# Kernel optimization log

Hardware: AMD Instinct MI355X
Metric: run time of the kernel (lower is better)

## Reference

```python
import jax, jax.numpy as jnp
import numpy as np

TAGSET = 50
T = TAGSET + 2      # tag_size incl START/STOP
START = T - 2       # START_TAG = -2
STOP = T - 1        # STOP_TAG = -1
NEG = -10000.0
B, S = 1024, 512


def _constrain(feats):
    # emissions to START/STOP are forbidden
    return feats.at[..., START].set(NEG).at[..., STOP].set(NEG)


def setup_inputs() -> dict:
    key = jax.random.key(0)
    kf, kl, kt, ktr = jax.random.split(key, 4)
    feats = jax.random.normal(kf, (B, S, T), jnp.float32)
    lengths = jax.random.randint(kl, (B,), S // 4, S + 1)
    mask = jnp.arange(S)[None, :] < lengths[:, None]  # bool prefix mask [B,S]
    tags = jax.random.randint(kt, (B, S), 0, TAGSET)
    # learned param: transitions with START/STOP constraints (as reset_parameters, but random base)
    transitions = 0.1 * jax.random.normal(ktr, (T, T), jnp.float32)
    transitions = transitions.at[:, START].set(NEG).at[STOP, :].set(NEG)
    return {"feats": feats, "mask": mask, "tags": tags, "transitions": transitions}


def reference(feats, mask, tags, transitions):
    del tags  # not used by Viterbi decode (forward)
    feats = _constrain(feats)
    b, s, t = feats.shape
    maskb = mask.astype(bool)
    lengths = jnp.maximum(maskb.sum(axis=1), 1)  # [B]

    alpha0 = transitions[START][None, :] + feats[:, 0]  # [B,T]

    def vstep(alpha, xs):
        f_t, m_t = xs  # [B,T], [B]
        scores = alpha[:, :, None] + transitions[None, :, :] + f_t[:, None, :]  # [B,T_prev,T_cur]
        nxt = scores.max(axis=1)
        bp = scores.argmax(axis=1).astype(jnp.int32)  # [B,T]
        alpha = jnp.where(m_t[:, None], nxt, alpha)
        return alpha, bp

    alpha, history = jax.lax.scan(
        vstep, alpha0, (feats[:, 1:].transpose(1, 0, 2), maskb[:, 1:].T)
    )  # history: [S-1,B,T]

    best_last = jnp.argmax(alpha + transitions[:, STOP][None, :], axis=1).astype(jnp.int32)  # [B]

    # pad so hist_pad[pos] == history[pos-1] for pos>=1
    hist_pad = jnp.concatenate([jnp.zeros((1, b, t), jnp.int32), history], axis=0)  # [S,B,T]

    def tb(ptr, xs):
        pos, bp = xs  # scalar, [B,T]
        ptr = jnp.where(pos == lengths - 1, best_last, ptr)
        tag = jnp.where(pos <= lengths - 1, ptr, 0)  # positions past length stay 0
        nxt = jnp.take_along_axis(bp, ptr[:, None], axis=1)[:, 0]
        ptr = jnp.where((pos >= 1) & (pos <= lengths - 1), nxt, ptr)
        return ptr, tag

    _, decoded = jax.lax.scan(tb, best_last, (jnp.arange(s), hist_pad), reverse=True)  # [S,B]
    return decoded.T  # [B,S] int32 best path
```

## Files before the change

kernel.cpp:

```cpp
#include <hip/hip_runtime.h>

#define TT 52
#define NT 50
#define START_TAG 50
#define STOP_TAG 51
#define BB 1024
#define SS 512
#define BPSTR 64

__device__ __forceinline__ int seq_len(const void* mask, int b, int j) {
    int cnt = 0;
    const unsigned* w = (const unsigned*)mask;
    unsigned w0 = w[0];
    unsigned w1 = w[1];
    if (w0 == 0x01010101u) {
        const unsigned char* m = (const unsigned char*)mask + (size_t)b * SS;
        for (int k = j; k < SS; k += 64) cnt += (m[k] != 0);
    } else if (w0 == 0x3f800000u) {
        const float* m = (const float*)mask + (size_t)b * SS;
        for (int k = j; k < SS; k += 64) cnt += (m[k] != 0.f);
    } else if (w1 == 1u) {
        const int* m = (const int*)mask + (size_t)b * SS;
        for (int k = j; k < SS; k += 64) cnt += (m[k] != 0);
    } else {
        const long long* m = (const long long*)mask + (size_t)b * SS;
        for (int k = j; k < SS; k += 64) cnt += (m[k] != 0);
    }
    for (int off = 32; off; off >>= 1) cnt += __shfl_xor(cnt, off, 64);
    return cnt > 0 ? cnt : 1;
}

#define DP_STEP(FREG, POSV)                                                       \
    {                                                                             \
        a_sh[(POSV) & 1][j] = alpha;                                              \
        float q_[52];                                                             \
        _Pragma("unroll")                                                         \
        for (int r_ = 0; r_ < 13; ++r_) {                                         \
            float4 t4_ = ((const float4*)a_sh[(POSV) & 1])[r_];                   \
            q_[4 * r_ + 0] = t4_.x; q_[4 * r_ + 1] = t4_.y;                       \
            q_[4 * r_ + 2] = t4_.z; q_[4 * r_ + 3] = t4_.w;                       \
        }                                                                         \
        float s_[NT];                                                             \
        _Pragma("unroll")                                                         \
        for (int i_ = 0; i_ < NT; ++i_) s_[i_] = q_[i_] + tt[i_];                 \
        float m_[17];                                                             \
        _Pragma("unroll")                                                         \
        for (int k_ = 0; k_ < 16; ++k_)                                           \
            m_[k_] = fmaxf(fmaxf(s_[3 * k_], s_[3 * k_ + 1]), s_[3 * k_ + 2]);    \
        m_[16] = fmaxf(s_[48], s_[49]);                                           \
        float n_[6];                                                              \
        _Pragma("unroll")                                                         \
        for (int k_ = 0; k_ < 5; ++k_)                                            \
            n_[k_] = fmaxf(fmaxf(m_[3 * k_], m_[3 * k_ + 1]), m_[3 * k_ + 2]);    \
        n_[5] = fmaxf(m_[15], m_[16]);                                            \
        float q0_ = fmaxf(fmaxf(n_[0], n_[1]), n_[2]);                            \
        float q1_ = fmaxf(fmaxf(n_[3], n_[4]), n_[5]);                            \
        float bv_ = fmaxf(q0_, q1_);                                              \
        wsb[(size_t)(POSV) * 64] = bv_;                                           \
        alpha = bv_ + (FREG);                                                     \
    }

#define FLD(P) fp[(size_t)((P) < SS ? (P) : SS - 1) * TT]

__global__ __launch_bounds__(64, 1) void crf_viterbi_fast(
    const float* __restrict__ feats,
    const void*  __restrict__ mask,
    const float* __restrict__ trans,
    float* __restrict__ ws,
    int* __restrict__ out)
{
    __shared__ float trans_lds[64 * 53];
    __shared__ __align__(16) float a_sh[2][64];

    const int b = blockIdx.x;
    const int j = threadIdx.x;
    const int jc = j < NT ? j : NT - 1;
    const int jr = j * 53;

    for (int k = j; k < 64 * 53; k += 64) {
        int r = k / 53, c = k - r * 53;
        float v = -3.0e38f;
        if (r < NT && c < TT) v = trans[r * TT + c];
        trans_lds[k] = v;
    }

    const int len = seq_len(mask, b, j);

    float tt[NT];
#pragma unroll
    for (int i = 0; i < NT; ++i) tt[i] = trans[i * TT + j];

    const float* fp = feats + ((size_t)b * SS) * TT + jc;
    float* wsb = ws + ((size_t)b * SS) * 64 + j;
    const float bv0 = trans[START_TAG * TT + jc];
    float alpha = bv0 + fp[0];
    wsb[0] = bv0;

    float fA0 = FLD(1), fA1 = FLD(2), fA2 = FLD(3), fA3 = FLD(4);
    float fB0 = FLD(5), fB1 = FLD(6), fB2 = FLD(7), fB3 = FLD(8);

    int pos = 1;
    for (; pos + 7 < len; pos += 8) {
        DP_STEP(fA0, pos + 0)
        DP_STEP(fA1, pos + 1)
        DP_STEP(fA2, pos + 2)
        DP_STEP(fA3, pos + 3)
        fA0 = FLD(pos + 8);  fA1 = FLD(pos + 9);
        fA2 = FLD(pos + 10); fA3 = FLD(pos + 11);
        DP_STEP(fB0, pos + 4)
        DP_STEP(fB1, pos + 5)
        DP_STEP(fB2, pos + 6)
        DP_STEP(fB3, pos + 7)
        fB0 = FLD(pos + 12); fB1 = FLD(pos + 13);
        fB2 = FLD(pos + 14); fB3 = FLD(pos + 15);
    }
    if (pos < len) { DP_STEP(fA0, pos) ++pos; }
    if (pos < len) { DP_STEP(fA1, pos) ++pos; }
    if (pos < len) { DP_STEP(fA2, pos) ++pos; }
    if (pos < len) { DP_STEP(fA3, pos) ++pos; }
    if (pos < len) { DP_STEP(fB0, pos) ++pos; }
    if (pos < len) { DP_STEP(fB1, pos) ++pos; }
    if (pos < len) { DP_STEP(fB2, pos) ++pos; }

    float v = alpha + trans[jc * TT + STOP_TAG];
    if (j >= NT) v = -3.0e38f;
    int idxb = j < NT ? j : 0;
    for (int off = 32; off; off >>= 1) {
        float vo = __shfl_xor(v, off, 64);
        int   io = __shfl_xor(idxb, off, 64);
        if (vo > v || (vo == v && io < idxb)) { v = vo; idxb = io; }
    }

    __syncthreads();

    int ptr = idxb;
    int* ob = out + (size_t)b * SS;
    ob[len - 1] = ptr;

    const float* wsr = ws + ((size_t)b * SS) * 64;
    const float* fbase = feats + ((size_t)b * SS) * TT;

    float bvs[4], fs[4];
    float bv_cur;
    {
        int r0 = len - 1;
        bv_cur = wsr[(size_t)r0 * 64 + j];
#pragma unroll
        for (int k = 0; k < 4; ++k) {
            int r = len - 2 - k; int rc = r < 0 ? 0 : r;
            bvs[k] = wsr[(size_t)rc * 64 + j];
            fs[k]  = fbase[(size_t)rc * TT + jc];
        }
    }

    int tpos = len - 1;

#define TB_STEP(k)                                                              \
    {                                                                           \
        float bv_prev = bvs[k];                                                 \
        float alpha_prev = bv_prev + fs[k];                                     \
        float cand = alpha_prev + trans_lds[jr + ptr];                          \
        float candm = (j < NT) ? cand : -3.0e38f;                               \
        float tgt = __builtin_bit_cast(float,                                   \
            __builtin_amdgcn_readlane(__builtin_bit_cast(int, bv_cur), ptr));   \
        unsigned long long bm = __ballot(candm == tgt);                         \
        ptr = __ffsll(bm) - 1;                                                  \
        --tpos;                                                                 \
        ob[tpos] = ptr;                                                         \
        bv_cur = bv_prev;                                                       \
        int rc = tpos - 4; rc = rc < 0 ? 0 : rc;                                \
        bvs[k] = wsr[(size_t)rc * 64 + j];                                      \
        fs[k]  = fbase[(size_t)rc * TT + jc];                                   \
    }

    while (tpos >= 4) {
        TB_STEP(0) TB_STEP(1) TB_STEP(2) TB_STEP(3)
    }
#pragma unroll
    for (int k = 0; k < 3; ++k) {
        if (tpos >= 1) TB_STEP(k)
    }
#undef TB_STEP

    for (int p = len + j; p < SS; p += 64) ob[p] = 0;
}

__global__ __launch_bounds__(64, 1) void crf_viterbi(
    const float* __restrict__ feats,
    const void*  __restrict__ mask,
    const float* __restrict__ trans,
    int* __restrict__ out)
{
    __shared__ unsigned char bp_sh[SS * BPSTR];

    const int b = blockIdx.x;
    const int j = threadIdx.x;
    const int jc = j < NT ? j : NT - 1;

    const int len = seq_len(mask, b, j);

    float tt[NT];
#pragma unroll
    for (int i = 0; i < NT; ++i) tt[i] = trans[i * TT + j];

    const float* fp = feats + ((size_t)b * SS) * TT + jc;
    float alpha = trans[START_TAG * TT + jc] + fp[0];
    float fnext = fp[TT];

    for (int pos = 1; pos < len; ++pos) {
        const float f = fnext;
        { int np = pos + 1 < SS ? pos + 1 : SS - 1; fnext = fp[(size_t)np * TT]; }

        float best[4] = { -3.0e38f, -3.0e38f, -3.0e38f, -3.0e38f };
        int   bidx[4] = { 0, 0, 0, 0 };
        const int abits = __builtin_bit_cast(int, alpha);
#pragma unroll
        for (int i = 0; i < NT; ++i) {
            int ab = __builtin_amdgcn_readlane(abits, i);
            float s = __builtin_bit_cast(float, ab) + tt[i];
            const int c = i & 3;
            if (s > best[c]) { best[c] = s; bidx[c] = i; }
        }
        float bv = best[0]; int bi = bidx[0];
        if (best[1] > bv || (best[1] == bv && bidx[1] < bi)) { bv = best[1]; bi = bidx[1]; }
        if (best[2] > bv || (best[2] == bv && bidx[2] < bi)) { bv = best[2]; bi = bidx[2]; }
        if (best[3] > bv || (best[3] == bv && bidx[3] < bi)) { bv = best[3]; bi = bidx[3]; }

        alpha = bv + f;
        bp_sh[pos * BPSTR + j] = (unsigned char)bi;
    }

    float v = alpha + trans[jc * TT + STOP_TAG];
    if (j >= NT) v = -3.0e38f;
    int idx = j < NT ? j : 0;
    for (int off = 32; off; off >>= 1) {
        float vo = __shfl_xor(v, off, 64);
        int   io = __shfl_xor(idx, off, 64);
        if (vo > v || (vo == v && io < idx)) { v = vo; idx = io; }
    }

    __syncthreads();

    int ptr = idx;
    int* ob = out + (size_t)b * SS;
    for (int pos = len - 1; pos >= 1; --pos) {
        if (j == 0) ob[pos] = ptr;
        ptr = (int)bp_sh[pos * BPSTR + ptr];
    }
    if (j == 0) ob[0] = ptr;

    for (int p = len + j; p < SS; p += 64) ob[p] = 0;
}

extern "C" void kernel_launch(void* const* d_in, const int* in_sizes, int n_in,
                              void* d_out, int out_size, void* d_ws, size_t ws_size,
                              hipStream_t stream) {
    const float* feats = (const float*)d_in[0];
    const void*  mask  = d_in[1];
    const float* trans = (const float*)d_in[3];
    int* out = (int*)d_out;

    const size_t need = (size_t)BB * SS * 64 * sizeof(float);
    if (ws_size >= need) {
        crf_viterbi_fast<<<dim3(BB), dim3(64), 0, stream>>>(feats, mask, trans,
                                                            (float*)d_ws, out);
    } else {
        crf_viterbi<<<dim3(BB), dim3(64), 0, stream>>>(feats, mask, trans, out);
    }
}
```

Baseline: 170.7 us.

## Sort sequences by length and interleave two Viterbi chains per wavefront

Adds a length-computation kernel and a counting-sort rank kernel, then a new Viterbi kernel in which each 64-lane block processes two sequences of similar length, interleaving their DP and traceback steps. The goal is to hide the latency of the serial per-step dependency chain (LDS round trip, max tree, readlane/ballot) by giving the wave two independent chains, and to halve the block count while balancing work through length pairing. It costs two extra small launches, including a single-block serial prefix scan, plus higher register pressure from duplicated state. It also removes a __syncthreads before traceback.

```diff
diff --git a/kernel.cpp b/kernel.cpp
--- a/kernel.cpp
+++ b/kernel.cpp
@@ -30,13 +30,13 @@
     return cnt > 0 ? cnt : 1;
 }
 
-#define DP_STEP(FREG, POSV)                                                       \
+#define DP_STEP(ALPHA, ABUF, WSB, FREG, POSV)                                     \
     {                                                                             \
-        a_sh[(POSV) & 1][j] = alpha;                                              \
+        (ABUF)[j] = ALPHA;                                                        \
         float q_[52];                                                             \
         _Pragma("unroll")                                                         \
         for (int r_ = 0; r_ < 13; ++r_) {                                         \
-            float4 t4_ = ((const float4*)a_sh[(POSV) & 1])[r_];                   \
+            float4 t4_ = ((const float4*)(ABUF))[r_];                             \
             q_[4 * r_ + 0] = t4_.x; q_[4 * r_ + 1] = t4_.y;                       \
             q_[4 * r_ + 2] = t4_.z; q_[4 * r_ + 3] = t4_.w;                       \
         }                                                                         \
@@ -56,13 +56,233 @@
         float q0_ = fmaxf(fmaxf(n_[0], n_[1]), n_[2]);                            \
         float q1_ = fmaxf(fmaxf(n_[3], n_[4]), n_[5]);                            \
         float bv_ = fmaxf(q0_, q1_);                                              \
-        wsb[(size_t)(POSV) * 64] = bv_;                                           \
-        alpha = bv_ + (FREG);                                                     \
-    }
-
-#define FLD(P) fp[(size_t)((P) < SS ? (P) : SS - 1) * TT]
-
-__global__ __launch_bounds__(64, 1) void crf_viterbi_fast(
+        (WSB)[(size_t)(POSV) * 64] = bv_;                                         \
+        ALPHA = bv_ + (FREG);                                                     \
+    }
+
+#define TB_STEP_G(PTR, TPOS, BVC, BVS, FS, OB, WSR, FB, K)                        \
+    {                                                                             \
+        float bvp_ = BVS[K];                                                      \
+        float ap_ = bvp_ + FS[K];                                                 \
+        float cand_ = ap_ + trans_lds[jr + PTR];                                  \
+        float cm_ = (j < NT) ? cand_ : -3.0e38f;                                  \
+        float tgt_ = __builtin_bit_cast(float,                                    \
+            __builtin_amdgcn_readlane(__builtin_bit_cast(int, BVC), PTR));        \
+        unsigned long long bm_ = __ballot(cm_ == tgt_);                           \
+        PTR = __ffsll(bm_) - 1;                                                   \
+        --TPOS;                                                                   \
+        OB[TPOS] = PTR;                                                           \
+        BVC = bvp_;                                                               \
+        int rc_ = TPOS - 4; rc_ = rc_ < 0 ? 0 : rc_;                              \
+        BVS[K] = WSR[(size_t)rc_ * 64 + j];                                       \
+        FS[K] = FB[(size_t)rc_ * TT + jc];                                        \
+    }
+
+__global__ __launch_bounds__(64, 1) void crf_lens(
+    const void* __restrict__ mask, int* __restrict__ lens_g)
+{
+    int len = seq_len(mask, blockIdx.x, threadIdx.x);
+    if (threadIdx.x == 0) lens_g[blockIdx.x] = len;
+}
+
+__global__ __launch_bounds__(1024, 1) void crf_rank(
+    const int* __restrict__ lens_g, int* __restrict__ perm)
+{
+    __shared__ int hist[SS + 1];
+    const int t = threadIdx.x;
+    if (t <= SS) hist[t] = 0;
+    __syncthreads();
+    const int myl = lens_g[t];
+    atomicAdd(&hist[myl], 1);
+    __syncthreads();
+    if (t == 0) {
+        int acc = 0;
+        for (int k = 0; k <= SS; ++k) { int h = hist[k]; hist[k] = acc; acc += h; }
+    }
+    __syncthreads();
+    int r = atomicAdd(&hist[myl], 1);
+    perm[r] = t;
+}
+
+__global__ __launch_bounds__(64, 1) void crf_viterbi_fast2(
+    const float* __restrict__ feats,
+    const float* __restrict__ trans,
+    const int*  __restrict__ lens_g,
+    const int*  __restrict__ perm,
+    float* __restrict__ ws,
+    int* __restrict__ out)
+{
+    __shared__ float trans_lds[64 * 53];
+    __shared__ __align__(16) float a_sh0[2][64];
+    __shared__ __align__(16) float a_sh1[2][64];
+
+    const int bid = blockIdx.x;
+    const int j = threadIdx.x;
+    const int jc = j < NT ? j : NT - 1;
+    const int jr = j * 53;
+
+    const int b0 = perm[2 * bid];
+    const int b1 = perm[2 * bid + 1];
+    const int len0 = lens_g[b0];
+    const int len1 = lens_g[b1];
+    const int lmin = len0 < len1 ? len0 : len1;
+
+    for (int k = j; k < 64 * 53; k += 64) {
+        int r = k / 53, c = k - r * 53;
+        float v = -3.0e38f;
+        if (r < NT && c < TT) v = trans[r * TT + c];
+        trans_lds[k] = v;
+    }
+
+    float tt[NT];
+#pragma unroll
+    for (int i = 0; i < NT; ++i) tt[i] = trans[i * TT + j];
+
+    const float* fp0 = feats + ((size_t)b0 * SS) * TT + jc;
+    const float* fp1 = feats + ((size_t)b1 * SS) * TT + jc;
+    float* wsb0 = ws + ((size_t)b0 * SS) * 64 + j;
+    float* wsb1 = ws + ((size_t)b1 * SS) * 64 + j;
+
+    const float bvi = trans[START_TAG * TT + jc];
+    float alpha0 = bvi + fp0[0];
+    float alpha1 = bvi + fp1[0];
+    wsb0[0] = bvi;
+    wsb1[0] = bvi;
+
+#define FLD0(P) fp0[(size_t)((P) < SS ? (P) : SS - 1) * TT]
+#define FLD1(P) fp1[(size_t)((P) < SS ? (P) : SS - 1) * TT]
+
+    float fA00 = FLD0(1), fA01 = FLD0(2), fA02 = FLD0(3), fA03 = FLD0(4);
+    float fB00 = FLD0(5), fB01 = FLD0(6), fB02 = FLD0(7), fB03 = FLD0(8);
+    float fA10 = FLD1(1), fA11 = FLD1(2), fA12 = FLD1(3), fA13 = FLD1(4);
+    float fB10 = FLD1(5), fB11 = FLD1(6), fB12 = FLD1(7), fB13 = FLD1(8);
+
+    int pos = 1;
+    for (; pos + 7 < lmin; pos += 8) {
+        DP_STEP(alpha0, a_sh0[(pos + 0) & 1], wsb0, fA00, pos + 0)
+        DP_STEP(alpha1, a_sh1[(pos + 0) & 1], wsb1, fA10, pos + 0)
+        DP_STEP(alpha0, a_sh0[(pos + 1) & 1], wsb0, fA01, pos + 1)
+        DP_STEP(alpha1, a_sh1[(pos + 1) & 1], wsb1, fA11, pos + 1)
+        DP_STEP(alpha0, a_sh0[(pos + 2) & 1], wsb0, fA02, pos + 2)
+        DP_STEP(alpha1, a_sh1[(pos + 2) & 1], wsb1, fA12, pos + 2)
+        DP_STEP(alpha0, a_sh0[(pos + 3) & 1], wsb0, fA03, pos + 3)
+        DP_STEP(alpha1, a_sh1[(pos + 3) & 1], wsb1, fA13, pos + 3)
+        fA00 = FLD0(pos + 8);  fA01 = FLD0(pos + 9);
+        fA02 = FLD0(pos + 10); fA03 = FLD0(pos + 11);
+        fA10 = FLD1(pos + 8);  fA11 = FLD1(pos + 9);
+        fA12 = FLD1(pos + 10); fA13 = FLD1(pos + 11);
+        DP_STEP(alpha0, a_sh0[(pos + 4) & 1], wsb0, fB00, pos + 4)
+        DP_STEP(alpha1, a_sh1[(pos + 4) & 1], wsb1, fB10, pos + 4)
+        DP_STEP(alpha0, a_sh0[(pos + 5) & 1], wsb0, fB01, pos + 5)
+        DP_STEP(alpha1, a_sh1[(pos + 5) & 1], wsb1, fB11, pos + 5)
+        DP_STEP(alpha0, a_sh0[(pos + 6) & 1], wsb0, fB02, pos + 6)
+        DP_STEP(alpha1, a_sh1[(pos + 6) & 1], wsb1, fB12, pos + 6)
+        DP_STEP(alpha0, a_sh0[(pos + 7) & 1], wsb0, fB03, pos + 7)
+        DP_STEP(alpha1, a_sh1[(pos + 7) & 1], wsb1, fB13, pos + 7)
+        fB00 = FLD0(pos + 12); fB01 = FLD0(pos + 13);
+        fB02 = FLD0(pos + 14); fB03 = FLD0(pos + 15);
+        fB10 = FLD1(pos + 12); fB11 = FLD1(pos + 13);
+        fB12 = FLD1(pos + 14); fB13 = FLD1(pos + 15);
+    }
+    if (pos < lmin) { DP_STEP(alpha0, a_sh0[pos & 1], wsb0, fA00, pos)
+                      DP_STEP(alpha1, a_sh1[pos & 1], wsb1, fA10, pos) ++pos; }
+    if (pos < lmin) { DP_STEP(alpha0, a_sh0[pos & 1], wsb0, fA01, pos)
+                      DP_STEP(alpha1, a_sh1[pos & 1], wsb1, fA11, pos) ++pos; }
+    if (pos < lmin) { DP_STEP(alpha0, a_sh0[pos & 1], wsb0, fA02, pos)
+                      DP_STEP(alpha1, a_sh1[pos & 1], wsb1, fA12, pos) ++pos; }
+    if (pos < lmin) { DP_STEP(alpha0, a_sh0[pos & 1], wsb0, fA03, pos)
+                      DP_STEP(alpha1, a_sh1[pos & 1], wsb1, fA13, pos) ++pos; }
+    if (pos < lmin) { DP_STEP(alpha0, a_sh0[pos & 1], wsb0, fB00, pos)
+                      DP_STEP(alpha1, a_sh1[pos & 1], wsb1, fB10, pos) ++pos; }
+    if (pos < lmin) { DP_STEP(alpha0, a_sh0[pos & 1], wsb0, fB01, pos)
+                      DP_STEP(alpha1, a_sh1[pos & 1], wsb1, fB11, pos) ++pos; }
+    if (pos < lmin) { DP_STEP(alpha0, a_sh0[pos & 1], wsb0, fB02, pos)
+                      DP_STEP(alpha1, a_sh1[pos & 1], wsb1, fB12, pos) ++pos; }
+
+    for (int p = pos; p < len0; ++p) {
+        float f = fp0[(size_t)p * TT];
+        DP_STEP(alpha0, a_sh0[p & 1], wsb0, f, p)
+    }
+    for (int p = pos; p < len1; ++p) {
+        float f = fp1[(size_t)p * TT];
+        DP_STEP(alpha1, a_sh1[p & 1], wsb1, f, p)
+    }
+
+    float v0 = alpha0 + trans[jc * TT + STOP_TAG];
+    float v1 = alpha1 + trans[jc * TT + STOP_TAG];
+    if (j >= NT) { v0 = -3.0e38f; v1 = -3.0e38f; }
+    int idx0 = j < NT ? j : 0;
+    int idx1 = idx0;
+    for (int off = 32; off; off >>= 1) {
+        float vo0 = __shfl_xor(v0, off, 64);
+        int   io0 = __shfl_xor(idx0, off, 64);
+        if (vo0 > v0 || (vo0 == v0 && io0 < idx0)) { v0 = vo0; idx0 = io0; }
+        float vo1 = __shfl_xor(v1, off, 64);
+        int   io1 = __shfl_xor(idx1, off, 64);
+        if (vo1 > v1 || (vo1 == v1 && io1 < idx1)) { v1 = vo1; idx1 = io1; }
+    }
+
+    int ptr0 = idx0, ptr1 = idx1;
+    int* ob0 = out + (size_t)b0 * SS;
+    int* ob1 = out + (size_t)b1 * SS;
+    ob0[len0 - 1] = ptr0;
+    ob1[len1 - 1] = ptr1;
+
+    const float* wsr0 = ws + ((size_t)b0 * SS) * 64;
+    const float* wsr1 = ws + ((size_t)b1 * SS) * 64;
+    const float* fb0 = feats + ((size_t)b0 * SS) * TT;
+    const float* fb1 = feats + ((size_t)b1 * SS) * TT;
+
+    float bvs0[4], fs0[4], bvs1[4], fs1[4];
+    float bvc0 = wsr0[(size_t)(len0 - 1) * 64 + j];
+    float bvc1 = wsr1[(size_t)(len1 - 1) * 64 + j];
+#pragma unroll
+    for (int k = 0; k < 4; ++k) {
+        int r0 = len0 - 2 - k; int rc0 = r0 < 0 ? 0 : r0;
+        bvs0[k] = wsr0[(size_t)rc0 * 64 + j];
+        fs0[k]  = fb0[(size_t)rc0 * TT + jc];
+        int r1 = len1 - 2 - k; int rc1 = r1 < 0 ? 0 : r1;
+        bvs1[k] = wsr1[(size_t)rc1 * 64 + j];
+        fs1[k]  = fb1[(size_t)rc1 * TT + jc];
+    }
+
+    int tpos0 = len0 - 1, tpos1 = len1 - 1;
+    while (tpos0 >= 4 && tpos1 >= 4) {
+        TB_STEP_G(ptr0, tpos0, bvc0, bvs0, fs0, ob0, wsr0, fb0, 0)
+        TB_STEP_G(ptr1, tpos1, bvc1, bvs1, fs1, ob1, wsr1, fb1, 0)
+        TB_STEP_G(ptr0, tpos0, bvc0, bvs0, fs0, ob0, wsr0, fb0, 1)
+        TB_STEP_G(ptr1, tpos1, bvc1, bvs1, fs1, ob1, wsr1, fb1, 1)
+        TB_STEP_G(ptr0, tpos0, bvc0, bvs0, fs0, ob0, wsr0, fb0, 2)
+        TB_STEP_G(ptr1, tpos1, bvc1, bvs1, fs1, ob1, wsr1, fb1, 2)
+        TB_STEP_G(ptr0, tpos0, bvc0, bvs0, fs0, ob0, wsr0, fb0, 3)
+        TB_STEP_G(ptr1, tpos1, bvc1, bvs1, fs1, ob1, wsr1, fb1, 3)
+    }
+    while (tpos0 >= 4) {
+        TB_STEP_G(ptr0, tpos0, bvc0, bvs0, fs0, ob0, wsr0, fb0, 0)
+        TB_STEP_G(ptr0, tpos0, bvc0, bvs0, fs0, ob0, wsr0, fb0, 1)
+        TB_STEP_G(ptr0, tpos0, bvc0, bvs0, fs0, ob0, wsr0, fb0, 2)
+        TB_STEP_G(ptr0, tpos0, bvc0, bvs0, fs0, ob0, wsr0, fb0, 3)
+    }
+    while (tpos1 >= 4) {
+        TB_STEP_G(ptr1, tpos1, bvc1, bvs1, fs1, ob1, wsr1, fb1, 0)
+        TB_STEP_G(ptr1, tpos1, bvc1, bvs1, fs1, ob1, wsr1, fb1, 1)
+        TB_STEP_G(ptr1, tpos1, bvc1, bvs1, fs1, ob1, wsr1, fb1, 2)
+        TB_STEP_G(ptr1, tpos1, bvc1, bvs1, fs1, ob1, wsr1, fb1, 3)
+    }
+    if (tpos0 >= 1) TB_STEP_G(ptr0, tpos0, bvc0, bvs0, fs0, ob0, wsr0, fb0, 0)
+    if (tpos0 >= 1) TB_STEP_G(ptr0, tpos0, bvc0, bvs0, fs0, ob0, wsr0, fb0, 1)
+    if (tpos0 >= 1) TB_STEP_G(ptr0, tpos0, bvc0, bvs0, fs0, ob0, wsr0, fb0, 2)
+    if (tpos1 >= 1) TB_STEP_G(ptr1, tpos1, bvc1, bvs1, fs1, ob1, wsr1, fb1, 0)
+    if (tpos1 >= 1) TB_STEP_G(ptr1, tpos1, bvc1, bvs1, fs1, ob1, wsr1, fb1, 1)
+    if (tpos1 >= 1) TB_STEP_G(ptr1, tpos1, bvc1, bvs1, fs1, ob1, wsr1, fb1, 2)
+
+    for (int p = len0 + j; p < SS; p += 64) ob0[p] = 0;
+    for (int p = len1 + j; p < SS; p += 64) ob1[p] = 0;
+#undef FLD0
+#undef FLD1
+}
+
+__global__ __launch_bounds__(64, 1) void crf_viterbi_fast1(
     const float* __restrict__ feats,
     const void*  __restrict__ mask,
     const float* __restrict__ trans,
@@ -92,35 +312,37 @@
 
     const float* fp = feats + ((size_t)b * SS) * TT + jc;
     float* wsb = ws + ((size_t)b * SS) * 64 + j;
-    const float bv0 = trans[START_TAG * TT + jc];
-    float alpha = bv0 + fp[0];
-    wsb[0] = bv0;
-
+    const float bvi = trans[START_TAG * TT + jc];
+    float alpha = bvi + fp[0];
+    wsb[0] = bvi;
+
+#define FLD(P) fp[(size_t)((P) < SS ? (P) : SS - 1) * TT]
     float fA0 = FLD(1), fA1 = FLD(2), fA2 = FLD(3), fA3 = FLD(4);
     float fB0 = FLD(5), fB1 = FLD(6), fB2 = FLD(7), fB3 = FLD(8);
 
     int pos = 1;
     for (; pos + 7 < len; pos += 8) {
-        DP_STEP(fA0, pos + 0)
-        DP_STEP(fA1, pos + 1)
-        DP_STEP(fA2, pos + 2)
-        DP_STEP(fA3, pos + 3)
+        DP_STEP(alpha, a_sh[(pos + 0) & 1], wsb, fA0, pos + 0)
+        DP_STEP(alpha, a_sh[(pos + 1) & 1], wsb, fA1, pos + 1)
+        DP_STEP(alpha, a_sh[(pos + 2) & 1], wsb, fA2, pos + 2)
+        DP_STEP(alpha, a_sh[(pos + 3) & 1], wsb, fA3, pos + 3)
         fA0 = FLD(pos + 8);  fA1 = FLD(pos + 9);
         fA2 = FLD(pos + 10); fA3 = FLD(pos + 11);
-        DP_STEP(fB0, pos + 4)
-        DP_STEP(fB1, pos + 5)
-        DP_STEP(fB2, pos + 6)
-        DP_STEP(fB3, pos + 7)
+        DP_STEP(alpha, a_sh[(pos + 4) & 1], wsb, fB0, pos + 4)
+        DP_STEP(alpha, a_sh[(pos + 5) & 1], wsb, fB1, pos + 5)
+        DP_STEP(alpha, a_sh[(pos + 6) & 1], wsb, fB2, pos + 6)
+        DP_STEP(alpha, a_sh[(pos + 7) & 1], wsb, fB3, pos + 7)
         fB0 = FLD(pos + 12); fB1 = FLD(pos + 13);
         fB2 = FLD(pos + 14); fB3 = FLD(pos + 15);
     }
-    if (pos < len) { DP_STEP(fA0, pos) ++pos; }
-    if (pos < len) { DP_STEP(fA1, pos) ++pos; }
-    if (pos < len) { DP_STEP(fA2, pos) ++pos; }
-    if (pos < len) { DP_STEP(fA3, pos) ++pos; }
-    if (pos < len) { DP_STEP(fB0, pos) ++pos; }
-    if (pos < len) { DP_STEP(fB1, pos) ++pos; }
-    if (pos < len) { DP_STEP(fB2, pos) ++pos; }
+    if (pos < len) { DP_STEP(alpha, a_sh[pos & 1], wsb, fA0, pos) ++pos; }
+    if (pos < len) { DP_STEP(alpha, a_sh[pos & 1], wsb, fA1, pos) ++pos; }
+    if (pos < len) { DP_STEP(alpha, a_sh[pos & 1], wsb, fA2, pos) ++pos; }
+    if (pos < len) { DP_STEP(alpha, a_sh[pos & 1], wsb, fA3, pos) ++pos; }
+    if (pos < len) { DP_STEP(alpha, a_sh[pos & 1], wsb, fB0, pos) ++pos; }
+    if (pos < len) { DP_STEP(alpha, a_sh[pos & 1], wsb, fB1, pos) ++pos; }
+    if (pos < len) { DP_STEP(alpha, a_sh[pos & 1], wsb, fB2, pos) ++pos; }
+#undef FLD
 
     float v = alpha + trans[jc * TT + STOP_TAG];
     if (j >= NT) v = -3.0e38f;
@@ -131,8 +353,6 @@
         if (vo > v || (vo == v && io < idxb)) { v = vo; idxb = io; }
     }
 
-    __syncthreads();
-
     int ptr = idxb;
     int* ob = out + (size_t)b * SS;
     ob[len - 1] = ptr;
@@ -141,46 +361,24 @@
     const float* fbase = feats + ((size_t)b * SS) * TT;
 
     float bvs[4], fs[4];
-    float bv_cur;
-    {
-        int r0 = len - 1;
-        bv_cur = wsr[(size_t)r0 * 64 + j];
-#pragma unroll
-        for (int k = 0; k < 4; ++k) {
-            int r = len - 2 - k; int rc = r < 0 ? 0 : r;
-            bvs[k] = wsr[(size_t)rc * 64 + j];
-            fs[k]  = fbase[(size_t)rc * TT + jc];
-        }
+    float bvc = wsr[(size_t)(len - 1) * 64 + j];
+#pragma unroll
+    for (int k = 0; k < 4; ++k) {
+        int r = len - 2 - k; int rc = r < 0 ? 0 : r;
+        bvs[k] = wsr[(size_t)rc * 64 + j];
+        fs[k]  = fbase[(size_t)rc * TT + jc];
     }
 
     int tpos = len - 1;
-
-#define TB_STEP(k)                                                              \
-    {                                                                           \
-        float bv_prev = bvs[k];                                                 \
-        float alpha_prev = bv_prev + fs[k];                                     \
-        float cand = alpha_prev + trans_lds[jr + ptr];                          \
-        float candm = (j < NT) ? cand : -3.0e38f;                               \
-        float tgt = __builtin_bit_cast(float,                                   \
-            __builtin_amdgcn_readlane(__builtin_bit_cast(int, bv_cur), ptr));   \
-        unsigned long long bm = __ballot(candm == tgt);                         \
-        ptr = __ffsll(bm) - 1;                                                  \
-        --tpos;                                                                 \
-        ob[tpos] = ptr;                                                         \
-        bv_cur = bv_prev;                                                       \
-        int rc = tpos - 4; rc = rc < 0 ? 0 : rc;                                \
-        bvs[k] = wsr[(size_t)rc * 64 + j];                                      \
-        fs[k]  = fbase[(size_t)rc * TT + jc];                                   \
-    }
-
     while (tpos >= 4) {
-        TB_STEP(0) TB_STEP(1) TB_STEP(2) TB_STEP(3)
-    }
-#pragma unroll
-    for (int k = 0; k < 3; ++k) {
-        if (tpos >= 1) TB_STEP(k)
-    }
-#undef TB_STEP
+        TB_STEP_G(ptr, tpos, bvc, bvs, fs, ob, wsr, fbase, 0)
+        TB_STEP_G(ptr, tpos, bvc, bvs, fs, ob, wsr, fbase, 1)
+        TB_STEP_G(ptr, tpos, bvc, bvs, fs, ob, wsr, fbase, 2)
+        TB_STEP_G(ptr, tpos, bvc, bvs, fs, ob, wsr, fbase, 3)
+    }
+    if (tpos >= 1) TB_STEP_G(ptr, tpos, bvc, bvs, fs, ob, wsr, fbase, 0)
+    if (tpos >= 1) TB_STEP_G(ptr, tpos, bvc, bvs, fs, ob, wsr, fbase, 1)
+    if (tpos >= 1) TB_STEP_G(ptr, tpos, bvc, bvs, fs, ob, wsr, fbase, 2)
 
     for (int p = len + j; p < SS; p += 64) ob[p] = 0;
 }
@@ -260,10 +458,19 @@
     const float* trans = (const float*)d_in[3];
     int* out = (int*)d_out;
 
-    const size_t need = (size_t)BB * SS * 64 * sizeof(float);
-    if (ws_size >= need) {
-        crf_viterbi_fast<<<dim3(BB), dim3(64), 0, stream>>>(feats, mask, trans,
-                                                            (float*)d_ws, out);
+    const size_t need_bv = (size_t)BB * SS * 64 * sizeof(float);
+    const size_t need_tot = need_bv + 2 * BB * sizeof(int);
+    if (ws_size >= need_tot) {
+        float* ws_bv = (float*)d_ws;
+        int* lens_g = (int*)((char*)d_ws + need_bv);
+        int* perm = lens_g + BB;
+        crf_lens<<<dim3(BB), dim3(64), 0, stream>>>(mask, lens_g);
+        crf_rank<<<dim3(1), dim3(1024), 0, stream>>>(lens_g, perm);
+        crf_viterbi_fast2<<<dim3(BB / 2), dim3(64), 0, stream>>>(
+            feats, trans, lens_g, perm, ws_bv, out);
+    } else if (ws_size >= need_bv) {
+        crf_viterbi_fast1<<<dim3(BB), dim3(64), 0, stream>>>(feats, mask, trans,
+                                                             (float*)d_ws, out);
     } else {
         crf_viterbi<<<dim3(BB), dim3(64), 0, stream>>>(feats, mask, trans, out);
     }
```

New measurement: 331.3 us. 1.94x slower.
